# Optimization experiments

Hardware: AMD Instinct MI355X
Metric: run time of the kernel (lower is better)

The kernel has to match this reference:

```python
import jax, jax.numpy as jnp
import numpy as np

L, D, V, BS, H, HD, DL = 12, 768, 50257, 1024, 12, 64, 256
B, T = 2, 1024
EPS = 1e-5


def _ln(x, w, b):
    m = jnp.mean(x, axis=-1, keepdims=True)
    v = jnp.mean((x - m) ** 2, axis=-1, keepdims=True)
    return (x - m) * jax.lax.rsqrt(v + EPS) * w + b


def _rope_tables(t_len):
    inv_freq = 1.0 / (10000.0 ** (jnp.arange(0, HD, 2, dtype=jnp.float32) / HD))
    t = jnp.arange(t_len, dtype=jnp.float32)
    freqs = jnp.outer(t, inv_freq)  # [T, HD/2]
    return jnp.cos(freqs), jnp.sin(freqs)


def _apply_rope(x, cos, sin):
    # x: [B, H, T, HD]; cos/sin: [T, HD/2]
    c = jnp.concatenate([cos, cos], axis=-1)[None, None]
    s = jnp.concatenate([sin, sin], axis=-1)[None, None]
    x1, x2 = jnp.split(x, 2, axis=-1)
    rot = jnp.concatenate([-x2, x1], axis=-1)
    return x * c + rot * s


def setup_inputs() -> dict:
    key = jax.random.key(0)
    ks = jax.random.split(key, 16)
    std = 0.02
    n = lambda k, shape: jax.random.normal(k, shape, dtype=jnp.float32) * std
    return {
        'idx': jax.random.randint(ks[0], (B, T), 0, V),
        'wte': n(ks[1], (V, D)),
        'wpe': n(ks[2], (BS, D)),
        'ln1_w': jnp.ones((L, D)), 'ln1_b': jnp.zeros((L, D)),
        'wq_w': n(ks[3], (L, D, H * HD)), 'wq_b': jnp.zeros((L, H * HD)),
        'kva_w': n(ks[4], (L, D, DL)), 'kva_b': jnp.zeros((L, DL)),
        'kvb_w': n(ks[5], (L, DL, 2 * H * HD)), 'kvb_b': jnp.zeros((L, 2 * H * HD)),
        'out_w': n(ks[6], (L, H * HD, D)), 'out_b': jnp.zeros((L, D)),
        'ln2_w': jnp.ones((L, D)), 'ln2_b': jnp.zeros((L, D)),
        'fc_w': n(ks[7], (L, D, 4 * D)), 'fc_b': jnp.zeros((L, 4 * D)),
        'proj_w': n(ks[8], (L, 4 * D, D)), 'proj_b': jnp.zeros((L, D)),
        'lnf_w': jnp.ones((D,)), 'lnf_b': jnp.zeros((D,)),
    }


def _forward(idx, wte, wpe, ln1_w, ln1_b, wq_w, wq_b, kva_w, kva_b, kvb_w, kvb_b,
             out_w, out_b, ln2_w, ln2_b, fc_w, fc_b, proj_w, proj_b, lnf_w, lnf_b):
    b, t = idx.shape
    x = wte[idx] + wpe[:t][None]  # [B,T,D]
    cos, sin = _rope_tables(t)
    scale = 1.0 / np.sqrt(HD)
    causal = jnp.tril(jnp.ones((t, t), dtype=bool))
    for l in range(L):
        h = _ln(x, ln1_w[l], ln1_b[l])
        q = (h @ wq_w[l] + wq_b[l]).reshape(b, t, H, HD).transpose(0, 2, 1, 3)
        kv_latent = h @ kva_w[l] + kva_b[l]  # [B,T,DL] (the cacheable latent)
        kv = (kv_latent @ kvb_w[l] + kvb_b[l]).reshape(b, t, 2, H, HD)
        kv = kv.transpose(2, 0, 3, 1, 4)  # [2,B,H,T,HD]
        k, v = kv[0], kv[1]
        q = _apply_rope(q, cos, sin)
        k = _apply_rope(k, cos, sin)
        scores = jnp.einsum('bhtd,bhsd->bhts', q, k) * scale
        scores = jnp.where(causal[None, None], scores, -jnp.inf)
        probs = jax.nn.softmax(scores, axis=-1)
        attn = jnp.einsum('bhts,bhsd->bhtd', probs, v)
        attn = attn.transpose(0, 2, 1, 3).reshape(b, t, H * HD)
        x = x + attn @ out_w[l] + out_b[l]
        h2 = _ln(x, ln2_w[l], ln2_b[l])
        mlp = jax.nn.gelu(h2 @ fc_w[l] + fc_b[l], approximate=False) @ proj_w[l] + proj_b[l]
        x = x + mlp
    x = _ln(x, lnf_w, lnf_b)
    logits = x @ wte.T  # tied lm_head
    return logits


def reference(idx, wte, wpe, ln1_w, ln1_b, wq_w, wq_b, kva_w, kva_b, kvb_w, kvb_b,
              out_w, out_b, ln2_w, ln2_b, fc_w, fc_b, proj_w, proj_b, lnf_w, lnf_b):
    return _forward(idx, wte, wpe, ln1_w, ln1_b, wq_w, wq_b, kva_w, kva_b, kvb_w,
                    kvb_b, out_w, out_b, ln2_w, ln2_b, fc_w, fc_b, proj_w, proj_b,
                    lnf_w, lnf_b)
```

## Files before the change

kernel.cpp:

```cpp
#include <hip/hip_runtime.h>
#include <cstdint>
#include <cstddef>


typedef unsigned short ushortT;
typedef __bf16 bf16x8 __attribute__((ext_vector_type(8)));
typedef float f32x4 __attribute__((ext_vector_type(4)));

#define NHEAD 12
#define T_SEQ 1024

__device__ __forceinline__ float bf2f(unsigned short u) {
    union { unsigned int i; float f; } v; v.i = ((unsigned int)u) << 16; return v.f;
}
__device__ __forceinline__ unsigned short f2bf(float f) {
    union { float f; unsigned int i; } v; v.f = f;
    unsigned int r = v.i + 0x7fffu + ((v.i >> 16) & 1u);
    return (unsigned short)(r >> 16);
}
__device__ __forceinline__ unsigned int pack2(float a, float b) {
    return (unsigned int)f2bf(a) | ((unsigned int)f2bf(b) << 16);
}
__device__ __forceinline__ void gload_lds16(const void* g, void* l) {
    __builtin_amdgcn_global_load_lds((__attribute__((address_space(1))) void*)g,
                                     (__attribute__((address_space(3))) void*)l, 16, 0, 0);
}
template <int N>
__device__ __forceinline__ void wait_vmcnt() {
    if constexpr (N == 8)      asm volatile("s_waitcnt vmcnt(8)" ::: "memory");
    else if constexpr (N == 6) asm volatile("s_waitcnt vmcnt(6)" ::: "memory");
    else if constexpr (N == 5) asm volatile("s_waitcnt vmcnt(5)" ::: "memory");
    else if constexpr (N == 4) asm volatile("s_waitcnt vmcnt(4)" ::: "memory");
    else                       asm volatile("s_waitcnt vmcnt(0)" ::: "memory");
}

__global__ __launch_bounds__(256) void transpose_cvt_kernel(
    const float* __restrict__ in, ushortT* __restrict__ outp,
    int K, int N, int outRowOff, size_t outLS) {
    __shared__ float tile[32][33];
    const int tid = threadIdx.x;
    const int n0 = blockIdx.x * 32, k0 = blockIdx.y * 32;
    const float* src = in + (size_t)blockIdx.z * K * N;
    {
        const int r = tid >> 3, cg = tid & 7;
        float4 v = *(const float4*)(src + (size_t)(k0 + r) * N + n0 + cg * 4);
        tile[r][cg * 4 + 0] = v.x; tile[r][cg * 4 + 1] = v.y;
        tile[r][cg * 4 + 2] = v.z; tile[r][cg * 4 + 3] = v.w;
    }
    __syncthreads();
    {
        const int nr = tid >> 3, kg = tid & 7;
        ushort4 o;
        o.x = f2bf(tile[kg * 4 + 0][nr]);
        o.y = f2bf(tile[kg * 4 + 1][nr]);
        o.z = f2bf(tile[kg * 4 + 2][nr]);
        o.w = f2bf(tile[kg * 4 + 3][nr]);
        ushortT* dst = outp + (size_t)blockIdx.z * outLS;
        *(ushort4*)(dst + (size_t)(outRowOff + n0 + nr) * K + k0 + kg * 4) = o;
    }
}

__global__ void cvt_wte_kernel(const float* __restrict__ in, ushortT* __restrict__ outp) {
    size_t i4 = (size_t)blockIdx.x * 256 + threadIdx.x;
    ushort4 o;
    if (i4 < 9649344) {
        float4 v = ((const float4*)in)[i4];
        o.x = f2bf(v.x); o.y = f2bf(v.y); o.z = f2bf(v.z); o.w = f2bf(v.w);
    } else { o.x = 0; o.y = 0; o.z = 0; o.w = 0; }
    ((ushort4*)outp)[i4] = o;
}

__global__ void embed_kernel(const int* __restrict__ idx, const float* __restrict__ wte,
                             const float* __restrict__ wpe, float* __restrict__ x) {
    int i = blockIdx.x * 256 + threadIdx.x;
    int row = i / 768, d = i - row * 768;
    int t = row & 1023;
    x[i] = wte[(size_t)idx[row] * 768 + d] + wpe[(size_t)t * 768 + d];
}

__global__ void rope_tables_kernel(float* __restrict__ cosT, float* __restrict__ sinT) {
    int i = blockIdx.x * 256 + threadIdx.x;
    int t = i >> 5, f = i & 31;
    float invf = exp2f(-(float)f * (13.287712379549449f / 32.0f));
    float ang = (float)t * invf;
    cosT[i] = cosf(ang);
    sinT[i] = sinf(ang);
}

__global__ __launch_bounds__(256) void ln_kernel(const float* __restrict__ x,
                                                 const float* __restrict__ wg,
                                                 const float* __restrict__ bg,
                                                 ushortT* __restrict__ outp) {
    const int row = blockIdx.x, tid = threadIdx.x;
    const float* xr = x + (size_t)row * 768;
    float v0 = xr[tid], v1 = xr[tid + 256], v2 = xr[tid + 512];
    float s = v0 + v1 + v2;
    float ss = v0 * v0 + v1 * v1 + v2 * v2;
#pragma unroll
    for (int off = 32; off >= 1; off >>= 1) {
        s += __shfl_xor(s, off);
        ss += __shfl_xor(ss, off);
    }
    __shared__ float sb[4], ssb[4];
    if ((tid & 63) == 0) { sb[tid >> 6] = s; ssb[tid >> 6] = ss; }
    __syncthreads();
    float S = sb[0] + sb[1] + sb[2] + sb[3];
    float SS = ssb[0] + ssb[1] + ssb[2] + ssb[3];
    const float mean = S * (1.0f / 768.0f);
    float var = SS * (1.0f / 768.0f) - mean * mean;
    const float rs = rsqrtf(var + 1e-5f);
    ushortT* orow = outp + (size_t)row * 768;
    orow[tid]       = f2bf((v0 - mean) * rs * wg[tid]       + bg[tid]);
    orow[tid + 256] = f2bf((v1 - mean) * rs * wg[tid + 256] + bg[tid + 256]);
    orow[tid + 512] = f2bf((v2 - mean) * rs * wg[tid + 512] + bg[tid + 512]);
}

template <int NP>
__global__ __launch_bounds__(256) void reduce_ln_kernel(
    float* __restrict__ x, const float* __restrict__ part,
    const float* __restrict__ bias,
    const float* __restrict__ wg, const float* __restrict__ bg,
    ushortT* __restrict__ outp) {
    const int row = blockIdx.x, tid = threadIdx.x;
    const size_t base = (size_t)row * 768;
    float4 v = {0.f, 0.f, 0.f, 0.f};
    if (tid < 192) {
        v = *(const float4*)(x + base + tid * 4);
        const float4 b4 = *(const float4*)(bias + tid * 4);
        v.x += b4.x; v.y += b4.y; v.z += b4.z; v.w += b4.w;
#pragma unroll
        for (int p = 0; p < NP; ++p) {
            const float4 pv = *(const float4*)(part + (size_t)p * 1572864 + base + tid * 4);
            v.x += pv.x; v.y += pv.y; v.z += pv.z; v.w += pv.w;
        }
        *(float4*)(x + base + tid * 4) = v;
    }
    float s = v.x + v.y + v.z + v.w;
    float ss = v.x * v.x + v.y * v.y + v.z * v.z + v.w * v.w;
#pragma unroll
    for (int off = 32; off >= 1; off >>= 1) {
        s += __shfl_xor(s, off);
        ss += __shfl_xor(ss, off);
    }
    __shared__ float sb[4], ssb[4];
    if ((tid & 63) == 0) { sb[tid >> 6] = s; ssb[tid >> 6] = ss; }
    __syncthreads();
    const float S = sb[0] + sb[1] + sb[2] + sb[3];
    const float SS = ssb[0] + ssb[1] + ssb[2] + ssb[3];
    const float mean = S * (1.0f / 768.0f);
    const float var = SS * (1.0f / 768.0f) - mean * mean;
    const float rs = rsqrtf(var + 1e-5f);
    if (tid < 192) {
        const float4 w4 = *(const float4*)(wg + tid * 4);
        const float4 g4 = *(const float4*)(bg + tid * 4);
        ushort4 o;
        o.x = f2bf((v.x - mean) * rs * w4.x + g4.x);
        o.y = f2bf((v.y - mean) * rs * w4.y + g4.y);
        o.z = f2bf((v.z - mean) * rs * w4.z + g4.z);
        o.w = f2bf((v.w - mean) * rs * w4.w + g4.w);
        *(ushort4*)(outp + base + tid * 4) = o;
    }
}

template <int BM, int NF, int NTHR, bool ROPE, bool PARTIAL = false>
__global__ __launch_bounds__(NTHR) void gemmT(
    const ushortT* __restrict__ A, int lda,
    const ushortT* __restrict__ Bt, int ldb,
    int K, int CS, int Nstore,
    const float* __restrict__ bias0, const float* __restrict__ bias1,
    ushortT* __restrict__ outB0, int ld0,
    ushortT* __restrict__ outB1, int ld1, int mode1,
    const float* __restrict__ resid, float* __restrict__ outF, int ldF,
    int act, const float* __restrict__ cosT, const float* __restrict__ sinT) {
    constexpr int WC = (NTHR == 512) ? 4 : 2;
    constexpr int WMR = BM / 2;
    constexpr int MF = WMR / 16;
    constexpr int NFh = NF / WC;
    constexpr int WNh = NFh * 16;
    constexpr int ABYTES = BM * 128;
    constexpr int BBYTES = NF * 2048;
    constexpr int BUFB = ABYTES + BBYTES;
    constexpr int A_LOADS = (BM * 8) / NTHR;
    constexpr int B_LOADS = (NF * 128) / NTHR;
    constexpr int S = A_LOADS + B_LOADS;
    __shared__ __align__(16) char lds[2 * BUFB];
    const int tid = threadIdx.x;
    const int w = tid >> 6, lane = tid & 63;
    const int wm = w / WC, wn = w % WC;
    const int gx = gridDim.x;
    const int nwg = gx * gridDim.y;
    const int flat = blockIdx.x + gx * blockIdx.y;
    const int xcd = flat & 7, loc = flat >> 3;
    const int qq = nwg >> 3, rr_ = nwg & 7;
    const int swz = (xcd < rr_ ? xcd * (qq + 1) : rr_ * (qq + 1) + (xcd - rr_) * qq) + loc;
    const int m0 = (swz % gx) * BM, n0 = (swz / gx) * NF * 16;
    const int fr = lane & 15, kg = lane >> 4;
    const size_t ldaB = (size_t)lda * 2, ldbB = (size_t)ldb * 2;
    int koff = 0;
    if constexpr (PARTIAL) koff = blockIdx.z * K;
    const char* Ab = (const char*)A + (size_t)koff * 2;
    const char* Bb = (const char*)Bt + (size_t)koff * 2;
    float* outFz = outF;
    if constexpr (PARTIAL) outFz = outF + (size_t)blockIdx.z * 2048 * (size_t)ldF;
    f32x4 acc[MF][NFh] = {};

    auto stage = [&](int buf, int t) {
        const size_t ktB = (size_t)t << 7;
        char* As_ = lds + buf * BUFB;
        char* Bs_ = As_ + ABYTES;
#pragma unroll
        for (int jj = 0; jj < A_LOADS; ++jj) {
            const int i = tid + jj * NTHR;
            const int r = i >> 3, c = i & 7, cc = c ^ (r & 7);
            gload_lds16(Ab + (size_t)(m0 + r) * ldaB + ktB + cc * 16, As_ + i * 16);
        }
#pragma unroll
        for (int jj = 0; jj < B_LOADS; ++jj) {
            const int i = tid + jj * NTHR;
            const int r = i >> 3, c = i & 7, cc = c ^ (r & 7);
            gload_lds16(Bb + (size_t)(n0 + r) * ldbB + ktB + cc * 16, Bs_ + i * 16);
        }
    };

    const int nk = K >> 6;
    stage(0, 0);
    if (nk > 1) { stage(1, 1); wait_vmcnt<S>(); }
    else        { wait_vmcnt<0>(); }
    __builtin_amdgcn_s_barrier();

    for (int t = 0; t < nk; ++t) {
        const int cur = t & 1;
        const char* As_ = lds + cur * BUFB;
        const char* Bs_ = As_ + ABYTES;
        bf16x8 af[MF][2], bfr[NFh][2];
#pragma unroll
        for (int mf = 0; mf < MF; ++mf) {
            const int row = wm * WMR + mf * 16 + fr;
#pragma unroll
            for (int ks = 0; ks < 2; ++ks)
                af[mf][ks] = *(const bf16x8*)(As_ + row * 128 + (((ks * 4 + kg) ^ (row & 7)) << 4));
        }
#pragma unroll
        for (int nf = 0; nf < NFh; ++nf) {
            const int row = wn * WNh + nf * 16 + fr;
#pragma unroll
            for (int ks = 0; ks < 2; ++ks)
                bfr[nf][ks] = *(const bf16x8*)(Bs_ + row * 128 + (((ks * 4 + kg) ^ (row & 7)) << 4));
        }
        if (t + 2 < nk) {
            asm volatile("s_waitcnt lgkmcnt(0)" ::: "memory");
            __builtin_amdgcn_s_barrier();
            stage(cur, t + 2);
        }
#pragma unroll
        for (int ks = 0; ks < 2; ++ks)
#pragma unroll
            for (int nf = 0; nf < NFh; ++nf)
#pragma unroll
                for (int mf = 0; mf < MF; ++mf)
                    acc[mf][nf] = __builtin_amdgcn_mfma_f32_16x16x32_bf16(
                        af[mf][ks], bfr[nf][ks], acc[mf][nf], 0, 0, 0);
        if (t + 1 < nk) {
            if (t + 2 < nk) wait_vmcnt<S>();
            else            wait_vmcnt<0>();
            __builtin_amdgcn_s_barrier();
        }
    }

    if constexpr (ROPE) {
        float vv[MF][4][4];
#pragma unroll
        for (int mf = 0; mf < MF; ++mf)
#pragma unroll
            for (int nf = 0; nf < 4; ++nf) {
                const int gcol = n0 + wn * 64 + nf * 16 + fr;
                float bv = (gcol < CS) ? (bias0 ? bias0[gcol] : 0.0f)
                                       : (bias1 ? bias1[gcol - CS] : 0.0f);
#pragma unroll
                for (int j = 0; j < 4; ++j) vv[mf][nf][j] = acc[mf][nf][j] + bv;
            }
        if (n0 + wn * 64 < 768) {
#pragma unroll
            for (int mf = 0; mf < MF; ++mf)
#pragma unroll
                for (int j = 0; j < 4; ++j) {
                    const int grow = m0 + wm * WMR + mf * 16 + kg * 4 + j;
                    const int t = grow & 1023;
                    const float c0 = cosT[t * 32 + fr],      s0 = sinT[t * 32 + fr];
                    const float c1 = cosT[t * 32 + 16 + fr], s1 = sinT[t * 32 + 16 + fr];
                    float x1 = vv[mf][0][j], x2 = vv[mf][2][j];
                    vv[mf][0][j] = x1 * c0 - x2 * s0;
                    vv[mf][2][j] = x2 * c0 + x1 * s0;
                    float y1 = vv[mf][1][j], y2 = vv[mf][3][j];
                    vv[mf][1][j] = y1 * c1 - y2 * s1;
                    vv[mf][3][j] = y2 * c1 + y1 * s1;
                }
        }
#pragma unroll
        for (int mf = 0; mf < MF; ++mf)
#pragma unroll
            for (int nf = 0; nf < 4; ++nf) {
                const int gcol = n0 + wn * 64 + nf * 16 + fr;
                if (gcol >= Nstore) continue;
#pragma unroll
                for (int j = 0; j < 4; ++j) {
                    const int grow = m0 + wm * WMR + mf * 16 + kg * 4 + j;
                    const float v = vv[mf][nf][j];
                    if (gcol < CS) {
                        if (outB0) outB0[(size_t)grow * ld0 + gcol] = f2bf(v);
                    } else if (outB1) {
                        if (mode1 == 0) {
                            outB1[(size_t)grow * ld1 + gcol - CS] = f2bf(v);
                        } else {
                            const int bb = grow >> 10, tt = grow & 1023;
                            const int hd = gcol - CS;
                            outB1[((size_t)((bb * 12 + (hd >> 6)) * 64 + (hd & 63)) << 10) + tt] = f2bf(v);
                        }
                    }
                }
            }
    } else {
#pragma unroll
        for (int mf = 0; mf < MF; ++mf) {
#pragma unroll
            for (int nf = 0; nf < NFh; ++nf) {
                const int gcol = n0 + wn * WNh + nf * 16 + fr;
                if (gcol >= Nstore) continue;
                float bv = 0.0f;
                if (gcol < CS) { if (bias0) bv = bias0[gcol]; }
                else           { if (bias1) bv = bias1[gcol - CS]; }
#pragma unroll
                for (int j = 0; j < 4; ++j) {
                    const int grow = m0 + wm * WMR + mf * 16 + kg * 4 + j;
                    float v = acc[mf][nf][j] + bv;
                    if (resid) v += resid[(size_t)grow * ldF + gcol];
                    if (act) v = 0.5f * v * (1.0f + erff(v * 0.70710678118654752f));
                    if (outFz) outFz[(size_t)grow * ldF + gcol] = v;
                    if (gcol < CS) {
                        if (outB0) outB0[(size_t)grow * ld0 + gcol] = f2bf(v);
                    } else if (outB1) {
                        if (mode1 == 0) {
                            outB1[(size_t)grow * ld1 + gcol - CS] = f2bf(v);
                        } else {
                            const int bb = grow >> 10, tt = grow & 1023;
                            const int hd = gcol - CS;
                            outB1[((size_t)((bb * 12 + (hd >> 6)) * 64 + (hd & 63)) << 10) + tt] = f2bf(v);
                        }
                    }
                }
            }
        }
    }
}

#define FC_PHASE(SLOT, MB, STAGE_STMT, TAILWAIT)                               \
    {                                                                          \
        bf16x8 af[2][2];                                                       \
        _Pragma("unroll") for (int m = 0; m < 2; ++m)                          \
        _Pragma("unroll") for (int ks = 0; ks < 2; ++ks) {                     \
            const int row = wm * 64 + (MB + m) * 16 + fr;                      \
            af[m][ks] = *(const bf16x8*)(lds + (SLOT) * 16384 + row * 128 +    \
                                         (((ks * 4 + kg) ^ (row & 7)) << 4));  \
        }                                                                      \
        STAGE_STMT;                                                            \
        __builtin_amdgcn_s_barrier();                                          \
        asm volatile("s_waitcnt lgkmcnt(0)" ::: "memory");                     \
        __builtin_amdgcn_sched_barrier(0);                                     \
        __builtin_amdgcn_s_setprio(1);                                         \
        _Pragma("unroll") for (int ks = 0; ks < 2; ++ks)                       \
        _Pragma("unroll") for (int nf = 0; nf < 4; ++nf)                       \
        _Pragma("unroll") for (int m = 0; m < 2; ++m)                          \
            acc[MB + m][nf] = __builtin_amdgcn_mfma_f32_16x16x32_bf16(         \
                af[m][ks], bfr[nf][ks], acc[MB + m][nf], 0, 0, 0);             \
        __builtin_amdgcn_s_setprio(0);                                         \
        TAILWAIT;                                                              \
        __builtin_amdgcn_s_barrier();                                          \
    }

template <bool GELU, bool PARTIAL>
__global__ __launch_bounds__(512, 1) void gemm8(
    const ushortT* __restrict__ A, int lda,
    const ushortT* __restrict__ Bt, int ldb,
    const float* __restrict__ bias,
    ushortT* __restrict__ outB, int ldo,
    float* __restrict__ outF) {
    __shared__ __align__(16) char lds[98304];
    const int tid = threadIdx.x;
    const int w = tid >> 6, lane = tid & 63;
    const int wm = w >> 2, wn = w & 3;
    const int fr = lane & 15, kg = lane >> 4;
    const int gx = gridDim.x;
    const int nwg = gx * gridDim.y;
    const int flat = blockIdx.x + gx * blockIdx.y;
    const int cpx = nwg >> 3;
    const int swz = (flat & 7) * cpx + (flat >> 3);
    const int m0 = (swz % gx) * 128, n0 = (swz / gx) * 256;
    const size_t ldaB = (size_t)lda * 2, ldbB = (size_t)ldb * 2;
    int koff = 0;
    if constexpr (PARTIAL) koff = blockIdx.z * 768;
    const char* Ag = (const char*)A + (size_t)koff * 2;
    const char* Bg = (const char*)Bt + (size_t)koff * 2;
    float* outFz = nullptr;
    if constexpr (PARTIAL) outFz = outF + (size_t)blockIdx.z * 2048 * 768;

    auto stA = [&](int tile) {
        char* dst = lds + (tile & 1) * 16384;
#pragma unroll
        for (int jj = 0; jj < 2; ++jj) {
            const int i = tid + jj * 512;
            const int r = i >> 3, c = i & 7, cc = c ^ (r & 7);
            gload_lds16(Ag + (size_t)(m0 + r) * ldaB + tile * 128 + cc * 16, dst + i * 16);
        }
    };
    auto stB = [&](int tile, int half) {
        char* dst = lds + 32768 + (tile & 1) * 32768 + half * 16384;
#pragma unroll
        for (int jj = 0; jj < 2; ++jj) {
            const int i = tid + jj * 512;
            const int r = i >> 3, c = i & 7, cc = c ^ (r & 7);
            gload_lds16(Bg + (size_t)(n0 + half * 128 + r) * ldbB + tile * 128 + cc * 16,
                        dst + i * 16);
        }
    };

    f32x4 acc[4][4] = {};
    stA(0); stB(0, 0); stB(0, 1); stB(1, 0); stB(1, 1);
    wait_vmcnt<4>();
    __builtin_amdgcn_s_barrier();

    const int browB = wn * 64;
    for (int i = 0; i < 6; ++i) {
        const int t1 = 2 * i + 1;
        const bool st = (i < 5);
        bf16x8 bfr[4][2];
#pragma unroll
        for (int nf = 0; nf < 4; ++nf)
#pragma unroll
            for (int ks = 0; ks < 2; ++ks) {
                const int row = browB + nf * 16 + fr;
                bfr[nf][ks] = *(const bf16x8*)(lds + 32768 + 0 * 32768 + row * 128 +
                                               (((ks * 4 + kg) ^ (row & 7)) << 4));
            }
        FC_PHASE(0, 0, stA(t1), )
        FC_PHASE(0, 2, if (st) { stB(t1 + 1, 0); stB(t1 + 1, 1); },
                 if (st) { wait_vmcnt<4>(); } else { wait_vmcnt<0>(); }
                 __builtin_amdgcn_sched_barrier(0))
#pragma unroll
        for (int nf = 0; nf < 4; ++nf)
#pragma unroll
            for (int ks = 0; ks < 2; ++ks) {
                const int row = browB + nf * 16 + fr;
                bfr[nf][ks] = *(const bf16x8*)(lds + 32768 + 1 * 32768 + row * 128 +
                                               (((ks * 4 + kg) ^ (row & 7)) << 4));
            }
        FC_PHASE(1, 0, if (st) stA(t1 + 1), )
        FC_PHASE(1, 2, if (st) { stB(t1 + 2, 0); stB(t1 + 2, 1); },
                 if (st) { wait_vmcnt<4>(); } else { wait_vmcnt<0>(); }
                 __builtin_amdgcn_sched_barrier(0))
    }

#pragma unroll
    for (int mf = 0; mf < 4; ++mf)
#pragma unroll
        for (int nf = 0; nf < 4; ++nf) {
            const int col = n0 + wn * 64 + nf * 16 + fr;
#pragma unroll
            for (int j = 0; j < 4; ++j) {
                const int row = m0 + wm * 64 + mf * 16 + kg * 4 + j;
                if constexpr (PARTIAL) {
                    outFz[(size_t)row * 768 + col] = acc[mf][nf][j];
                } else {
                    float v = acc[mf][nf][j] + bias[col];
                    if constexpr (GELU)
                        v = 0.5f * v * (1.0f + erff(v * 0.70710678118654752f));
                    outB[(size_t)row * ldo + col] = f2bf(v);
                }
            }
        }
}

#define LM_PHASE(SLOT, MB, STAGE_STMT, TAILWAIT)                              \
    {                                                                          \
        bf16x8 af[2][2];                                                       \
        _Pragma("unroll") for (int m = 0; m < 2; ++m)                          \
        _Pragma("unroll") for (int ks = 0; ks < 2; ++ks) {                     \
            const int row = (MB + m) * 16 + fr;                                \
            af[m][ks] = *(const bf16x8*)(Aw + (SLOT) * 32768 + row * 128 +     \
                                         (((ks * 4 + kg) ^ (row & 7)) << 4));  \
        }                                                                      \
        STAGE_STMT;                                                            \
        __builtin_amdgcn_s_barrier();                                          \
        asm volatile("s_waitcnt lgkmcnt(0)" ::: "memory");                     \
        __builtin_amdgcn_sched_barrier(0);                                     \
        __builtin_amdgcn_s_setprio(1);                                         \
        _Pragma("unroll") for (int ks = 0; ks < 2; ++ks)                       \
        _Pragma("unroll") for (int nf = 0; nf < 4; ++nf)                       \
        _Pragma("unroll") for (int m = 0; m < 2; ++m)                          \
            acc[MB + m][nf] = __builtin_amdgcn_mfma_f32_16x16x32_bf16(         \
                af[m][ks], bfr[nf][ks], acc[MB + m][nf], 0, 0, 0);             \
        __builtin_amdgcn_s_setprio(0);                                         \
        TAILWAIT;                                                              \
        __builtin_amdgcn_s_barrier();                                          \
    }

__global__ __launch_bounds__(512, 1) void lmhead8(
    const ushortT* __restrict__ A, const ushortT* __restrict__ Bt,
    float* __restrict__ outF) {
    __shared__ __align__(16) char lds[131072];
    const int tid = threadIdx.x;
    const int w = tid >> 6, lane = tid & 63;
    const int wm = w >> 2, wn = w & 3;
    const int fr = lane & 15, kg = lane >> 4;
    const int flat = blockIdx.x + 8 * blockIdx.y;
    const int swz = (flat & 7) * 197 + (flat >> 3);
    const int m0 = (swz & 7) * 256, n0 = (swz >> 3) * 256;

    const char* Ag = (const char*)A;
    const char* Bg = (const char*)Bt;
    const char* Aw = lds + wm * 16384;
    const char* Bw = lds + 65536 + (wn >> 1) * 16384;
    const int brow0 = (wn & 1) * 64;

    auto stA = [&](int tile, int half) {
        char* dst = lds + (tile & 1) * 32768 + half * 16384;
#pragma unroll
        for (int jj = 0; jj < 2; ++jj) {
            const int i = tid + jj * 512;
            const int r = i >> 3, c = i & 7, cc = c ^ (r & 7);
            gload_lds16(Ag + (size_t)(m0 + half * 128 + r) * 1536 + tile * 128 + cc * 16,
                        dst + i * 16);
        }
    };
    auto stB = [&](int tile, int half) {
        char* dst = lds + 65536 + (tile & 1) * 32768 + half * 16384;
#pragma unroll
        for (int jj = 0; jj < 2; ++jj) {
            const int i = tid + jj * 512;
            const int r = i >> 3, c = i & 7, cc = c ^ (r & 7);
            gload_lds16(Bg + (size_t)(n0 + half * 128 + r) * 1536 + tile * 128 + cc * 16,
                        dst + i * 16);
        }
    };

    f32x4 acc[8][4] = {};
    stA(0, 0); stA(0, 1); stB(0, 0); stB(0, 1); stB(1, 0); stB(1, 1);
    wait_vmcnt<4>();
    __builtin_amdgcn_s_barrier();

    for (int i = 0; i < 6; ++i) {
        const int t1 = 2 * i + 1;
        const bool st = (i < 5);
        bf16x8 bfr[4][2];
#pragma unroll
        for (int nf = 0; nf < 4; ++nf)
#pragma unroll
            for (int ks = 0; ks < 2; ++ks) {
                const int row = brow0 + nf * 16 + fr;
                bfr[nf][ks] = *(const bf16x8*)(Bw + 0 * 32768 + row * 128 +
                                               (((ks * 4 + kg) ^ (row & 7)) << 4));
            }
        LM_PHASE(0, 0, stA(t1, 0), )
        LM_PHASE(0, 2, stA(t1, 1), )
        LM_PHASE(0, 4, if (st) stB(t1 + 1, 0), )
        LM_PHASE(0, 6, if (st) stB(t1 + 1, 1),
                 if (st) { wait_vmcnt<4>(); } else { wait_vmcnt<0>(); }
                 __builtin_amdgcn_sched_barrier(0))
#pragma unroll
        for (int nf = 0; nf < 4; ++nf)
#pragma unroll
            for (int ks = 0; ks < 2; ++ks) {
                const int row = brow0 + nf * 16 + fr;
                bfr[nf][ks] = *(const bf16x8*)(Bw + 1 * 32768 + row * 128 +
                                               (((ks * 4 + kg) ^ (row & 7)) << 4));
            }
        LM_PHASE(1, 0, if (st) stA(t1 + 1, 0), )
        LM_PHASE(1, 2, if (st) stA(t1 + 1, 1), )
        LM_PHASE(1, 4, if (st) stB(t1 + 2, 0), )
        LM_PHASE(1, 6, if (st) stB(t1 + 2, 1),
                 if (st) { wait_vmcnt<4>(); } else { wait_vmcnt<0>(); }
                 __builtin_amdgcn_sched_barrier(0))
    }

#pragma unroll
    for (int mf = 0; mf < 8; ++mf)
#pragma unroll
        for (int nf = 0; nf < 4; ++nf) {
            const int col = n0 + wn * 64 + nf * 16 + fr;
            if (col < 50257) {
#pragma unroll
                for (int j = 0; j < 4; ++j) {
                    const int row = m0 + wm * 128 + mf * 16 + kg * 4 + j;
                    outF[(size_t)row * 50257 + col] = acc[mf][nf][j];
                }
            }
        }
}

__global__ __launch_bounds__(256) void attn_mfma(const ushortT* __restrict__ q,
                                                 const ushortT* __restrict__ kbuf,
                                                 const ushortT* __restrict__ vT,
                                                 ushortT* __restrict__ attnb) {
    __shared__ __align__(16) char lds[41472];
    const int tid = threadIdx.x, w = tid >> 6, lane = tid & 63;
    const int fr = lane & 15, kg = lane >> 4;
    const int flat = blockIdx.x + 16 * blockIdx.y;
    const int nf2 = (flat & 7) * 48 + (flat >> 3);
    const int bh = nf2 >> 4;
    const int b = bh / NHEAD, h = bh % NHEAD;
    const int qb = (15 - (nf2 & 15)) * 64;
    const int q0 = qb + w * 16;
    const int nst = (qb >> 6) + 1, diag = qb >> 6;

    const ushortT* qrow = q + ((size_t)(b * 1024 + q0 + fr) * 768 + h * 64);
    const bf16x8 qf0 = *(const bf16x8*)(qrow + kg * 8);
    const bf16x8 qf1 = *(const bf16x8*)(qrow + 32 + kg * 8);

    const char* kgb = (const char*)kbuf + ((size_t)(b * 1024) * 768 + h * 64) * 2;
    const char* vgb = (const char*)vT + ((size_t)(b * 12 + h) * 65536) * 2;
    char* Pw = lds + 32768 + w * 2176 + fr * 136;

    auto stage = [&](int buf, int st) {
#pragma unroll
        for (int jj = 0; jj < 2; ++jj) {
            const int i = tid + jj * 256;
            const int r = i >> 3, c = i & 7, cc = c ^ (r & 7);
            gload_lds16(kgb + (size_t)(st * 64 + r) * 1536 + cc * 16, lds + buf * 8192 + i * 16);
            gload_lds16(vgb + (size_t)r * 2048 + st * 128 + cc * 16, lds + 16384 + buf * 8192 + i * 16);
        }
    };

    float m_r = -1e30f, l_r = 0.0f;
    f32x4 o[4] = {};

    stage(0, 0);
    if (nst > 1) stage(1, 1);
    for (int st = 0; st < nst; ++st) {
        const int cur = st & 1;
        if (st + 1 < nst) wait_vmcnt<4>();
        else              wait_vmcnt<0>();
        __builtin_amdgcn_s_barrier();
        const char* Kd = lds + cur * 8192;
        const char* Vd = lds + 16384 + cur * 8192;

        f32x4 sfr[4];
        __builtin_amdgcn_s_setprio(1);
#pragma unroll
        for (int n = 0; n < 4; ++n) {
            const int row = n * 16 + fr;
            bf16x8 k0 = *(const bf16x8*)(Kd + row * 128 + ((kg ^ (row & 7)) << 4));
            bf16x8 k1 = *(const bf16x8*)(Kd + row * 128 + (((4 + kg) ^ (row & 7)) << 4));
            f32x4 sa = {0.0f, 0.0f, 0.0f, 0.0f};
            sa = __builtin_amdgcn_mfma_f32_16x16x32_bf16(k0, qf0, sa, 0, 0, 0);
            sa = __builtin_amdgcn_mfma_f32_16x16x32_bf16(k1, qf1, sa, 0, 0, 0);
            sfr[n] = sa;
        }
        __builtin_amdgcn_s_setprio(0);
        const int qoff = w * 16 + fr;
#pragma unroll
        for (int n = 0; n < 4; ++n)
#pragma unroll
            for (int j = 0; j < 4; ++j) {
                float v = sfr[n][j] * 0.125f;
                if (st == diag && (n * 16 + kg * 4 + j) > qoff) v = -1e30f;
                sfr[n][j] = v;
            }
        float tm = -1e30f;
#pragma unroll
        for (int n = 0; n < 4; ++n)
#pragma unroll
            for (int j = 0; j < 4; ++j) tm = fmaxf(tm, sfr[n][j]);
        tm = fmaxf(tm, __shfl_xor(tm, 16));
        tm = fmaxf(tm, __shfl_xor(tm, 32));
        const float mnew = fmaxf(m_r, tm);
        const float fac = __expf(m_r - mnew);
        m_r = mnew;
        l_r *= fac;
        const float ff0 = __shfl(fac, kg * 4 + 0);
        const float ff1 = __shfl(fac, kg * 4 + 1);
        const float ff2 = __shfl(fac, kg * 4 + 2);
        const float ff3 = __shfl(fac, kg * 4 + 3);
#pragma unroll
        for (int nf = 0; nf < 4; ++nf) {
            o[nf][0] *= ff0; o[nf][1] *= ff1; o[nf][2] *= ff2; o[nf][3] *= ff3;
        }
#pragma unroll
        for (int n = 0; n < 4; ++n) {
            float e0 = __expf(sfr[n][0] - mnew);
            float e1 = __expf(sfr[n][1] - mnew);
            float e2 = __expf(sfr[n][2] - mnew);
            float e3 = __expf(sfr[n][3] - mnew);
            l_r += (e0 + e1) + (e2 + e3);
            uint2 pv;
            pv.x = pack2(e0, e1);
            pv.y = pack2(e2, e3);
            *(uint2*)(Pw + n * 32 + kg * 8) = pv;
        }
        __builtin_amdgcn_s_setprio(1);
#pragma unroll
        for (int ks = 0; ks < 2; ++ks) {
            uint2 a0 = *(const uint2*)(Pw + ks * 64 + kg * 16);
            uint2 a1 = *(const uint2*)(Pw + ks * 64 + kg * 16 + 8);
            union { uint4 u; bf16x8 v; } pa;
            pa.u = make_uint4(a0.x, a0.y, a1.x, a1.y);
#pragma unroll
            for (int nf = 0; nf < 4; ++nf) {
                const int row = nf * 16 + fr;
                bf16x8 vf = *(const bf16x8*)(Vd + row * 128 + (((ks * 4 + kg) ^ (row & 7)) << 4));
                o[nf] = __builtin_amdgcn_mfma_f32_16x16x32_bf16(pa.v, vf, o[nf], 0, 0, 0);
            }
        }
        __builtin_amdgcn_s_setprio(0);
        __builtin_amdgcn_s_barrier();
        if (st + 2 < nst) stage(cur, st + 2);
    }

    l_r += __shfl_xor(l_r, 16);
    l_r += __shfl_xor(l_r, 32);
    const float inv = 1.0f / l_r;
    const float iv0 = __shfl(inv, kg * 4 + 0);
    const float iv1 = __shfl(inv, kg * 4 + 1);
    const float iv2 = __shfl(inv, kg * 4 + 2);
    const float iv3 = __shfl(inv, kg * 4 + 3);
#pragma unroll
    for (int nf = 0; nf < 4; ++nf) {
        const size_t base = (size_t)(b * 1024 + q0) * 768 + h * 64 + nf * 16 + fr;
        attnb[base + (size_t)(kg * 4 + 0) * 768] = f2bf(o[nf][0] * iv0);
        attnb[base + (size_t)(kg * 4 + 1) * 768] = f2bf(o[nf][1] * iv1);
        attnb[base + (size_t)(kg * 4 + 2) * 768] = f2bf(o[nf][2] * iv2);
        attnb[base + (size_t)(kg * 4 + 3) * 768] = f2bf(o[nf][3] * iv3);
    }
}

extern "C" void kernel_launch(void* const* d_in, const int* in_sizes, int n_in,
                              void* d_out, int out_size, void* d_ws, size_t ws_size,
                              hipStream_t stream) {
    (void)in_sizes; (void)n_in; (void)out_size; (void)ws_size;
    const int*   idxp   = (const int*)d_in[0];
    const float* wte    = (const float*)d_in[1];
    const float* wpe    = (const float*)d_in[2];
    const float* ln1_w  = (const float*)d_in[3];
    const float* ln1_b  = (const float*)d_in[4];
    const float* wq_w   = (const float*)d_in[5];
    const float* wq_b   = (const float*)d_in[6];
    const float* kva_w  = (const float*)d_in[7];
    const float* kva_b  = (const float*)d_in[8];
    const float* kvb_w  = (const float*)d_in[9];
    const float* kvb_b  = (const float*)d_in[10];
    const float* out_w  = (const float*)d_in[11];
    const float* out_b  = (const float*)d_in[12];
    const float* ln2_w  = (const float*)d_in[13];
    const float* ln2_b  = (const float*)d_in[14];
    const float* fc_w   = (const float*)d_in[15];
    const float* fc_b   = (const float*)d_in[16];
    const float* proj_w = (const float*)d_in[17];
    const float* proj_b = (const float*)d_in[18];
    const float* lnf_w  = (const float*)d_in[19];
    const float* lnf_b  = (const float*)d_in[20];

    char* ws = (char*)d_ws;
    size_t off = 0;
    auto alloc = [&](size_t bytes) -> char* {
        char* p = ws + off;
        off += (bytes + 255) & ~(size_t)255;
        return p;
    };
    ushortT* wqkvaT = (ushortT*)alloc((size_t)12 * 1024 * 768 * 2);
    ushortT* kvbT   = (ushortT*)alloc((size_t)12 * 1536 * 256 * 2);
    ushortT* outT   = (ushortT*)alloc((size_t)12 * 768 * 768 * 2);
    ushortT* fcT    = (ushortT*)alloc((size_t)12 * 3072 * 768 * 2);
    ushortT* projT  = (ushortT*)alloc((size_t)12 * 768 * 3072 * 2);
    ushortT* wteB   = (ushortT*)alloc((size_t)50432 * 768 * 2);
    float* cosT = (float*)alloc((size_t)1024 * 32 * 4);
    float* sinT = (float*)alloc((size_t)1024 * 32 * 4);
    float*   x     = (float*)alloc((size_t)2048 * 768 * 4);
    ushortT* h     = (ushortT*)alloc((size_t)2048 * 768 * 2);
    ushortT* qbuf  = (ushortT*)alloc((size_t)2048 * 768 * 2);
    ushortT* lat   = (ushortT*)alloc((size_t)2048 * 256 * 2);
    ushortT* kvbuf = (ushortT*)alloc((size_t)2048 * 768 * 2);
    ushortT* vTb   = (ushortT*)alloc((size_t)24 * 64 * 1024 * 2);
    ushortT* attnb = (ushortT*)alloc((size_t)2048 * 768 * 2);
    ushortT* fca   = (ushortT*)alloc((size_t)2048 * 3072 * 2);
    float*   partB = (float*)alloc((size_t)4 * 2048 * 768 * 4);

    transpose_cvt_kernel<<<dim3(24, 24, 12), 256, 0, stream>>>(wq_w,  wqkvaT, 768, 768,  0,   (size_t)1024 * 768);
    transpose_cvt_kernel<<<dim3(8,  24, 12), 256, 0, stream>>>(kva_w, wqkvaT, 768, 256,  768, (size_t)1024 * 768);
    transpose_cvt_kernel<<<dim3(48, 8,  12), 256, 0, stream>>>(kvb_w, kvbT,   256, 1536, 0,   (size_t)1536 * 256);
    transpose_cvt_kernel<<<dim3(24, 24, 12), 256, 0, stream>>>(out_w, outT,   768, 768,  0,   (size_t)768 * 768);
    transpose_cvt_kernel<<<dim3(96, 24, 12), 256, 0, stream>>>(fc_w,  fcT,    768, 3072, 0,   (size_t)3072 * 768);
    transpose_cvt_kernel<<<dim3(24, 96, 12), 256, 0, stream>>>(proj_w, projT, 3072, 768, 0,   (size_t)768 * 3072);
    cvt_wte_kernel<<<37824, 256, 0, stream>>>(wte, wteB);
    rope_tables_kernel<<<128, 256, 0, stream>>>(cosT, sinT);
    embed_kernel<<<6144, 256, 0, stream>>>(idxp, wte, wpe, x);
    ln_kernel<<<2048, 256, 0, stream>>>(x, ln1_w, ln1_b, h);

    for (int l = 0; l < 12; ++l) {
        gemmT<64, 8, 256, true><<<dim3(32, 8), 256, 0, stream>>>(
            h, 768, wqkvaT + (size_t)l * 1024 * 768, 768,
            768, 768, 1024, wq_b + l * 768, kva_b + l * 256,
            qbuf, 768, lat, 256, 0, nullptr, nullptr, 0, 0, cosT, sinT);
        gemmT<64, 8, 256, true><<<dim3(32, 12), 256, 0, stream>>>(
            lat, 256, kvbT + (size_t)l * 1536 * 256, 256,
            256, 768, 1536, kvb_b + l * 1536, kvb_b + l * 1536 + 768,
            kvbuf, 768, vTb, 0, 1, nullptr, nullptr, 0, 0, cosT, sinT);
        attn_mfma<<<dim3(16, 24), 256, 0, stream>>>(qbuf, kvbuf, vTb, attnb);
        gemmT<64, 8, 256, false, true><<<dim3(32, 6, 2), 256, 0, stream>>>(
            attnb, 768, outT + (size_t)l * 768 * 768, 768,
            384, 768, 768, nullptr, nullptr,
            nullptr, 0, nullptr, 0, 0, nullptr, partB, 768, 0, nullptr, nullptr);
        reduce_ln_kernel<2><<<2048, 256, 0, stream>>>(
            x, partB, out_b + l * 768, ln2_w + l * 768, ln2_b + l * 768, h);
        gemm8<true, false><<<dim3(16, 12), 512, 0, stream>>>(
            h, 768, fcT + (size_t)l * 3072 * 768, 768,
            fc_b + l * 3072, fca, 3072, nullptr);
        gemm8<false, true><<<dim3(16, 3, 4), 512, 0, stream>>>(
            fca, 3072, projT + (size_t)l * 768 * 3072, 3072,
            nullptr, nullptr, 0, partB);
        const float* nw = (l < 11) ? ln1_w + (l + 1) * 768 : lnf_w;
        const float* nb = (l < 11) ? ln1_b + (l + 1) * 768 : lnf_b;
        reduce_ln_kernel<4><<<2048, 256, 0, stream>>>(
            x, partB, proj_b + l * 768, nw, nb, h);
    }
    lmhead8<<<dim3(8, 197), 512, 0, stream>>>(h, wteB, (float*)d_out);
}
```

Baseline: 1.819 ms.

## Narrow MLP GEMM N-tile to 192 and add lazy softmax rescaling in attention

The MLP GEMM kernel gets an NFW template parameter, shrinking each workgroup's N tile from 256 to 192 columns. That cuts B-tile LDS use and raises the grid from 192/192 to 256/256 workgroups for the FC and projection GEMMs, which should fill the CUs better. Separately, the flash-attention inner loop skips the running-max update and output rescale unless some row's new max exceeds the old one by more than 8. That removes exp and shuffle work on most tiles, at the cost of carrying larger unnormalized exponent values.

```diff
diff --git a/kernel.cpp b/kernel.cpp
--- a/kernel.cpp
+++ b/kernel.cpp
@@ -31,6 +31,7 @@
     else if constexpr (N == 6) asm volatile("s_waitcnt vmcnt(6)" ::: "memory");
     else if constexpr (N == 5) asm volatile("s_waitcnt vmcnt(5)" ::: "memory");
     else if constexpr (N == 4) asm volatile("s_waitcnt vmcnt(4)" ::: "memory");
+    else if constexpr (N == 3) asm volatile("s_waitcnt vmcnt(3)" ::: "memory");
     else                       asm volatile("s_waitcnt vmcnt(0)" ::: "memory");
 }
 
@@ -368,7 +369,7 @@
         __builtin_amdgcn_sched_barrier(0);                                     \
         __builtin_amdgcn_s_setprio(1);                                         \
         _Pragma("unroll") for (int ks = 0; ks < 2; ++ks)                       \
-        _Pragma("unroll") for (int nf = 0; nf < 4; ++nf)                       \
+        _Pragma("unroll") for (int nf = 0; nf < NFW; ++nf)                     \
         _Pragma("unroll") for (int m = 0; m < 2; ++m)                          \
             acc[MB + m][nf] = __builtin_amdgcn_mfma_f32_16x16x32_bf16(         \
                 af[m][ks], bfr[nf][ks], acc[MB + m][nf], 0, 0, 0);             \
@@ -377,14 +378,15 @@
         __builtin_amdgcn_s_barrier();                                          \
     }
 
-template <bool GELU, bool PARTIAL>
+template <int NFW, bool GELU, bool PARTIAL>
 __global__ __launch_bounds__(512, 1) void gemm8(
     const ushortT* __restrict__ A, int lda,
     const ushortT* __restrict__ Bt, int ldb,
     const float* __restrict__ bias,
     ushortT* __restrict__ outB, int ldo,
     float* __restrict__ outF) {
-    __shared__ __align__(16) char lds[98304];
+    constexpr int BSLOT = NFW * 8192;
+    __shared__ __align__(16) char lds[32768 + 2 * BSLOT];
     const int tid = threadIdx.x;
     const int w = tid >> 6, lane = tid & 63;
     const int wm = w >> 2, wn = w & 3;
@@ -394,7 +396,7 @@
     const int flat = blockIdx.x + gx * blockIdx.y;
     const int cpx = nwg >> 3;
     const int swz = (flat & 7) * cpx + (flat >> 3);
-    const int m0 = (swz % gx) * 128, n0 = (swz / gx) * 256;
+    const int m0 = (swz % gx) * 128, n0 = (swz / gx) * (NFW * 64);
     const size_t ldaB = (size_t)lda * 2, ldbB = (size_t)ldb * 2;
     int koff = 0;
     if constexpr (PARTIAL) koff = blockIdx.z * 768;
@@ -412,58 +414,57 @@
             gload_lds16(Ag + (size_t)(m0 + r) * ldaB + tile * 128 + cc * 16, dst + i * 16);
         }
     };
-    auto stB = [&](int tile, int half) {
-        char* dst = lds + 32768 + (tile & 1) * 32768 + half * 16384;
-#pragma unroll
-        for (int jj = 0; jj < 2; ++jj) {
+    auto stB = [&](int tile) {
+        char* dst = lds + 32768 + (tile & 1) * BSLOT;
+#pragma unroll
+        for (int jj = 0; jj < NFW; ++jj) {
             const int i = tid + jj * 512;
             const int r = i >> 3, c = i & 7, cc = c ^ (r & 7);
-            gload_lds16(Bg + (size_t)(n0 + half * 128 + r) * ldbB + tile * 128 + cc * 16,
-                        dst + i * 16);
+            gload_lds16(Bg + (size_t)(n0 + r) * ldbB + tile * 128 + cc * 16, dst + i * 16);
         }
     };
 
-    f32x4 acc[4][4] = {};
-    stA(0); stB(0, 0); stB(0, 1); stB(1, 0); stB(1, 1);
-    wait_vmcnt<4>();
+    f32x4 acc[4][NFW] = {};
+    stA(0); stB(0); stB(1);
+    wait_vmcnt<NFW>();
     __builtin_amdgcn_s_barrier();
 
-    const int browB = wn * 64;
+    const int browB = wn * (NFW * 16);
     for (int i = 0; i < 6; ++i) {
         const int t1 = 2 * i + 1;
         const bool st = (i < 5);
-        bf16x8 bfr[4][2];
-#pragma unroll
-        for (int nf = 0; nf < 4; ++nf)
+        bf16x8 bfr[NFW][2];
+#pragma unroll
+        for (int nf = 0; nf < NFW; ++nf)
 #pragma unroll
             for (int ks = 0; ks < 2; ++ks) {
                 const int row = browB + nf * 16 + fr;
-                bfr[nf][ks] = *(const bf16x8*)(lds + 32768 + 0 * 32768 + row * 128 +
+                bfr[nf][ks] = *(const bf16x8*)(lds + 32768 + 0 * BSLOT + row * 128 +
                                                (((ks * 4 + kg) ^ (row & 7)) << 4));
             }
         FC_PHASE(0, 0, stA(t1), )
-        FC_PHASE(0, 2, if (st) { stB(t1 + 1, 0); stB(t1 + 1, 1); },
-                 if (st) { wait_vmcnt<4>(); } else { wait_vmcnt<0>(); }
+        FC_PHASE(0, 2, if (st) stB(t1 + 1),
+                 if (st) { wait_vmcnt<NFW>(); } else { wait_vmcnt<0>(); }
                  __builtin_amdgcn_sched_barrier(0))
 #pragma unroll
-        for (int nf = 0; nf < 4; ++nf)
+        for (int nf = 0; nf < NFW; ++nf)
 #pragma unroll
             for (int ks = 0; ks < 2; ++ks) {
                 const int row = browB + nf * 16 + fr;
-                bfr[nf][ks] = *(const bf16x8*)(lds + 32768 + 1 * 32768 + row * 128 +
+                bfr[nf][ks] = *(const bf16x8*)(lds + 32768 + 1 * BSLOT + row * 128 +
                                                (((ks * 4 + kg) ^ (row & 7)) << 4));
             }
         FC_PHASE(1, 0, if (st) stA(t1 + 1), )
-        FC_PHASE(1, 2, if (st) { stB(t1 + 2, 0); stB(t1 + 2, 1); },
-                 if (st) { wait_vmcnt<4>(); } else { wait_vmcnt<0>(); }
+        FC_PHASE(1, 2, if (st) stB(t1 + 2),
+                 if (st) { wait_vmcnt<NFW>(); } else { wait_vmcnt<0>(); }
                  __builtin_amdgcn_sched_barrier(0))
     }
 
 #pragma unroll
     for (int mf = 0; mf < 4; ++mf)
 #pragma unroll
-        for (int nf = 0; nf < 4; ++nf) {
-            const int col = n0 + wn * 64 + nf * 16 + fr;
+        for (int nf = 0; nf < NFW; ++nf) {
+            const int col = n0 + wn * (NFW * 16) + nf * 16 + fr;
 #pragma unroll
             for (int j = 0; j < 4; ++j) {
                 const int row = m0 + wm * 64 + mf * 16 + kg * 4 + j;
@@ -671,24 +672,26 @@
             for (int j = 0; j < 4; ++j) tm = fmaxf(tm, sfr[n][j]);
         tm = fmaxf(tm, __shfl_xor(tm, 16));
         tm = fmaxf(tm, __shfl_xor(tm, 32));
-        const float mnew = fmaxf(m_r, tm);
-        const float fac = __expf(m_r - mnew);
-        m_r = mnew;
-        l_r *= fac;
-        const float ff0 = __shfl(fac, kg * 4 + 0);
-        const float ff1 = __shfl(fac, kg * 4 + 1);
-        const float ff2 = __shfl(fac, kg * 4 + 2);
-        const float ff3 = __shfl(fac, kg * 4 + 3);
-#pragma unroll
-        for (int nf = 0; nf < 4; ++nf) {
-            o[nf][0] *= ff0; o[nf][1] *= ff1; o[nf][2] *= ff2; o[nf][3] *= ff3;
+        if (!__all(tm <= m_r + 8.0f)) {
+            const float mnew = fmaxf(m_r, tm);
+            const float fac = __expf(m_r - mnew);
+            m_r = mnew;
+            l_r *= fac;
+            const float ff0 = __shfl(fac, kg * 4 + 0);
+            const float ff1 = __shfl(fac, kg * 4 + 1);
+            const float ff2 = __shfl(fac, kg * 4 + 2);
+            const float ff3 = __shfl(fac, kg * 4 + 3);
+#pragma unroll
+            for (int nf = 0; nf < 4; ++nf) {
+                o[nf][0] *= ff0; o[nf][1] *= ff1; o[nf][2] *= ff2; o[nf][3] *= ff3;
+            }
         }
 #pragma unroll
         for (int n = 0; n < 4; ++n) {
-            float e0 = __expf(sfr[n][0] - mnew);
-            float e1 = __expf(sfr[n][1] - mnew);
-            float e2 = __expf(sfr[n][2] - mnew);
-            float e3 = __expf(sfr[n][3] - mnew);
+            float e0 = __expf(sfr[n][0] - m_r);
+            float e1 = __expf(sfr[n][1] - m_r);
+            float e2 = __expf(sfr[n][2] - m_r);
+            float e3 = __expf(sfr[n][3] - m_r);
             l_r += (e0 + e1) + (e2 + e3);
             uint2 pv;
             pv.x = pack2(e0, e1);
@@ -809,10 +812,10 @@
             nullptr, 0, nullptr, 0, 0, nullptr, partB, 768, 0, nullptr, nullptr);
         reduce_ln_kernel<2><<<2048, 256, 0, stream>>>(
             x, partB, out_b + l * 768, ln2_w + l * 768, ln2_b + l * 768, h);
-        gemm8<true, false><<<dim3(16, 12), 512, 0, stream>>>(
+        gemm8<3, true, false><<<dim3(16, 16), 512, 0, stream>>>(
             h, 768, fcT + (size_t)l * 3072 * 768, 768,
             fc_b + l * 3072, fca, 3072, nullptr);
-        gemm8<false, true><<<dim3(16, 3, 4), 512, 0, stream>>>(
+        gemm8<3, false, true><<<dim3(16, 4, 4), 512, 0, stream>>>(
             fca, 3072, projT + (size_t)l * 768 * 3072, 3072,
             nullptr, nullptr, 0, partB);
         const float* nw = (l < 11) ? ln1_w + (l + 1) * 768 : lnf_w;
```

Measured after the change: 1.738 ms (median of 3 runs). 1.05x faster.
